# Kernel tuning notes

Measured on AMD Instinct MI355X. Metric: run time of the kernel, lower is better.

The kernel has to match this reference:

```python
import jax, jax.numpy as jnp
import numpy as np

Z_DIM = 1          # coord column zeroed before coalescing (module default)
GRID = 512         # max coordinate value per column (exclusive)


def setup_inputs() -> dict:
    key = jax.random.key(0)
    k1, k2 = jax.random.split(key)
    N, C = 400000, 128
    features = jax.random.normal(k1, (N, C), dtype=jnp.float32)
    coords = jax.random.randint(k2, (N, 4), 0, GRID, dtype=jnp.int32)
    return {"features": features, "coords": coords}


def reference(features, coords):
    # features: [N, C] float, coords: [N, 4] int32
    N = features.shape[0]
    # Zero the z column (BEV flattening), as in flatten_coords[:, z_dim] = 0.
    # Since the z column is identically 0 after zeroing, coalescing the 4-col
    # coords is equivalent to keying on the remaining 3 columns.
    non_z = [i for i in range(4) if i != Z_DIM]
    c0 = coords[:, non_z[0]].astype(jnp.int32)
    c1 = coords[:, non_z[1]].astype(jnp.int32)
    c2 = coords[:, non_z[2]].astype(jnp.int32)
    lin_key = (c0 * GRID + c1) * GRID + c2  # < 512^3 < 2^31, fits int32

    # coalesce(): unique coords + scatter-add of [count | features]
    uniq, inv = jnp.unique(lin_key, size=N, fill_value=-1, return_inverse=True)
    ones = jnp.ones((N, 1), dtype=features.dtype)
    feat_with_cnt = jnp.concatenate([ones, features], axis=1)  # [N, C+1]
    sums = jax.ops.segment_sum(feat_with_cnt, inv.reshape(-1), num_segments=N)  # [N, C+1]

    cnt = sums[:, :1]
    out_features = sums[:, 1:] / jnp.maximum(cnt, 1.0)  # padded rows have cnt=0 -> stay 0

    # Decode unique keys back to 4-column coords (z column = 0).
    d2 = uniq % GRID
    rem = uniq // GRID
    d1 = rem % GRID
    d0 = rem // GRID
    zeros = jnp.zeros_like(d0)
    cols = [None] * 4
    cols[Z_DIM] = zeros
    cols[non_z[0]] = d0
    cols[non_z[1]] = d1
    cols[non_z[2]] = d2
    out_coords = jnp.stack(cols, axis=1).astype(jnp.int32)  # [N, 4], padded rows negative

    return out_features, out_coords, cnt[:, 0]
```

## Files before the change

kernel.cpp:

```cpp
#include <hip/hip_runtime.h>


#define NWORDS      (1u << 22)
#define SCAN_BLOCKS 1024
#define WPB         (NWORDS / SCAN_BLOCKS)
#define WPT         (WPB / 256)

__device__ __forceinline__ unsigned key_of(const int* __restrict__ coords, int i) {
    int c0 = coords[(size_t)i * 4 + 0];
    int c1 = coords[(size_t)i * 4 + 2];
    int c2 = coords[(size_t)i * 4 + 3];
    return ((unsigned)c0 << 18) | ((unsigned)c1 << 9) | (unsigned)c2;
}

__global__ void k_build(const int* __restrict__ coords, unsigned* __restrict__ bitmap, int N) {
    int i = blockIdx.x * blockDim.x + threadIdx.x;
    if (i >= N) return;
    unsigned key = key_of(coords, i);
    atomicOr(&bitmap[key >> 5], 1u << (key & 31u));
}

__global__ void k_scan1(const unsigned* __restrict__ bitmap, unsigned* __restrict__ blockSums) {
    __shared__ unsigned sd[256];
    const uint4* bm = (const uint4*)(bitmap + (size_t)blockIdx.x * WPB + (size_t)threadIdx.x * WPT);
    unsigned s = 0;
#pragma unroll
    for (int k = 0; k < WPT / 4; ++k) {
        uint4 v = bm[k];
        s += __popc(v.x) + __popc(v.y) + __popc(v.z) + __popc(v.w);
    }
    sd[threadIdx.x] = s;
    __syncthreads();
    for (int off = 128; off > 0; off >>= 1) {
        if ((int)threadIdx.x < off) sd[threadIdx.x] += sd[threadIdx.x + off];
        __syncthreads();
    }
    if (threadIdx.x == 0) blockSums[blockIdx.x] = sd[0];
}

__global__ void k_scan2(const unsigned* __restrict__ blockSums, unsigned* __restrict__ blockOffsets) {
    __shared__ unsigned sd[SCAN_BLOCKS];
    int t = threadIdx.x;
    unsigned v = blockSums[t];
    sd[t] = v;
    __syncthreads();
    for (int off = 1; off < SCAN_BLOCKS; off <<= 1) {
        unsigned add = (t >= off) ? sd[t - off] : 0u;
        __syncthreads();
        sd[t] += add;
        __syncthreads();
    }
    blockOffsets[t] = sd[t] - v;
}

__global__ void k_scan3(const unsigned* __restrict__ bitmap,
                        const unsigned* __restrict__ blockOffsets,
                        unsigned* __restrict__ offsets) {
    __shared__ unsigned sd[256];
    size_t base = (size_t)blockIdx.x * WPB + (size_t)threadIdx.x * WPT;
    const uint4* bm = (const uint4*)(bitmap + base);
    unsigned pc[WPT];
    unsigned s = 0;
#pragma unroll
    for (int k = 0; k < WPT / 4; ++k) {
        uint4 v = bm[k];
        pc[k * 4 + 0] = __popc(v.x);
        pc[k * 4 + 1] = __popc(v.y);
        pc[k * 4 + 2] = __popc(v.z);
        pc[k * 4 + 3] = __popc(v.w);
        s += pc[k * 4] + pc[k * 4 + 1] + pc[k * 4 + 2] + pc[k * 4 + 3];
    }
    int t = threadIdx.x;
    sd[t] = s;
    __syncthreads();
    for (int off = 1; off < 256; off <<= 1) {
        unsigned add = (t >= off) ? sd[t - off] : 0u;
        __syncthreads();
        sd[t] += add;
        __syncthreads();
    }
    unsigned run = blockOffsets[blockIdx.x] + sd[t] - s;
#pragma unroll
    for (int k = 0; k < WPT; ++k) {
        offsets[base + k] = run;
        run += pc[k];
    }
}

__global__ void k_fill(float4* __restrict__ outc, int N) {
    int i = blockIdx.x * blockDim.x + threadIdx.x;
    if (i >= N) return;
    outc[i] = make_float4(-1.f, 0.f, 511.f, 511.f);
}

__global__ void k_enum(const unsigned* __restrict__ bitmap,
                       const unsigned* __restrict__ offsets,
                       float4* __restrict__ outc) {
    unsigned w = blockIdx.x * blockDim.x + threadIdx.x;
    unsigned bits = bitmap[w];
    if (!bits) return;
    unsigned row = offsets[w];
    while (bits) {
        int b = __ffs(bits) - 1;
        unsigned key = (w << 5) | (unsigned)b;
        float d0 = (float)(key >> 18);
        float d1 = (float)((key >> 9) & 511u);
        float d2 = (float)(key & 511u);
        outc[row] = make_float4(d0, 0.f, d1, d2);
        ++row;
        bits &= bits - 1u;
    }
}

__global__ void k_seg(const int* __restrict__ coords,
                      const unsigned* __restrict__ bitmap,
                      const unsigned* __restrict__ offsets,
                      unsigned* __restrict__ seg,
                      float* __restrict__ cnt, int N) {
    int i = blockIdx.x * blockDim.x + threadIdx.x;
    if (i >= N) return;
    unsigned key = key_of(coords, i);
    unsigned w = key >> 5, b = key & 31u;
    unsigned s = offsets[w] + __popc(bitmap[w] & ((1u << b) - 1u));
    seg[i] = s;
    atomicAdd(&cnt[s], 1.0f);
}

__global__ void k_zero(const float* __restrict__ cnt, float4* __restrict__ feat, int N) {
    int r = blockIdx.x * blockDim.x + threadIdx.x;
    if (r >= N) return;
    if (cnt[r] != 1.0f) {
        float4 z = make_float4(0.f, 0.f, 0.f, 0.f);
#pragma unroll
        for (int k = 0; k < 32; ++k) feat[(size_t)r * 32 + k] = z;
    }
}

__global__ void k_scatter(const float4* __restrict__ fin,
                          const unsigned* __restrict__ seg,
                          const float* __restrict__ cnt,
                          float4* __restrict__ fout, int N) {
    int gid = blockIdx.x * blockDim.x + threadIdx.x;
    int elem = gid >> 5;
    int c4 = gid & 31;
    if (elem >= N) return;
    unsigned s = seg[elem];
    float cv = cnt[s];
    float4 v = fin[(size_t)elem * 32 + c4];
    if (cv == 1.0f) {
        fout[(size_t)s * 32 + c4] = v;
    } else {
        float inv = 1.0f / cv;
        float* p = (float*)&fout[(size_t)s * 32 + c4];
        atomicAdd(p + 0, v.x * inv);
        atomicAdd(p + 1, v.y * inv);
        atomicAdd(p + 2, v.z * inv);
        atomicAdd(p + 3, v.w * inv);
    }
}

extern "C" void kernel_launch(void* const* d_in, const int* in_sizes, int n_in,
                              void* d_out, int out_size, void* d_ws, size_t ws_size,
                              hipStream_t stream) {
    const float4* feat_in = (const float4*)d_in[0];
    const int* coords = (const int*)d_in[1];
    int N = in_sizes[1] / 4;

    float* out = (float*)d_out;
    float* out_feat = out;
    float4* out_coords = (float4*)(out + (size_t)N * 128);
    float* out_cnt = out + (size_t)N * 132;

    unsigned* bitmap = (unsigned*)d_out;
    unsigned* offsets = bitmap + NWORDS;

    unsigned* seg = (unsigned*)d_ws;
    unsigned* blockSums = seg + N;
    unsigned* blockOffsets = blockSums + SCAN_BLOCKS;

    int nb = (N + 255) / 256;

    hipMemsetAsync(bitmap, 0, (size_t)NWORDS * 4, stream);
    hipMemsetAsync(out_cnt, 0, (size_t)N * 4, stream);

    k_build<<<nb, 256, 0, stream>>>(coords, bitmap, N);
    k_scan1<<<SCAN_BLOCKS, 256, 0, stream>>>(bitmap, blockSums);
    k_scan2<<<1, SCAN_BLOCKS, 0, stream>>>(blockSums, blockOffsets);
    k_scan3<<<SCAN_BLOCKS, 256, 0, stream>>>(bitmap, blockOffsets, offsets);
    k_fill<<<nb, 256, 0, stream>>>(out_coords, N);
    k_enum<<<NWORDS / 256, 256, 0, stream>>>(bitmap, offsets, out_coords);
    k_seg<<<nb, 256, 0, stream>>>(coords, bitmap, offsets, seg, out_cnt, N);
    k_zero<<<nb, 256, 0, stream>>>(out_cnt, (float4*)out_feat, N);
    k_scatter<<<(int)(((size_t)N * 32 + 255) / 256), 256, 0, stream>>>(
        feat_in, seg, out_cnt, (float4*)out_feat, N);
}
```

Before: 168.7 us.

## Fuse enumeration into scan, replace scatter with gather plus duplicate atomics

Fuses the coordinate enumeration into the final scan kernel and drops the separate fill kernel. Padding coords are now written inside the new gather kernel, using a total-unique count saved by the second scan. Keys are cached during the build pass, and an inverse map from unique row to source element lets singleton rows be copied by a coalesced gather. Only duplicate rows still use per-element atomic adds, now one thread per element looping over channels. The bitmap and offsets move from the output buffer to the workspace, which needs a larger workspace. The rewrite removes the zeroing pass and the full scatter, at the cost of an extra dependent pass over the output.

```diff
diff --git a/kernel.cpp b/kernel.cpp
--- a/kernel.cpp
+++ b/kernel.cpp
@@ -13,10 +13,12 @@
     return ((unsigned)c0 << 18) | ((unsigned)c1 << 9) | (unsigned)c2;
 }
 
-__global__ void k_build(const int* __restrict__ coords, unsigned* __restrict__ bitmap, int N) {
+__global__ void k_build(const int* __restrict__ coords, unsigned* __restrict__ bitmap,
+                        unsigned* __restrict__ keys, int N) {
     int i = blockIdx.x * blockDim.x + threadIdx.x;
     if (i >= N) return;
     unsigned key = key_of(coords, i);
+    keys[i] = key;
     atomicOr(&bitmap[key >> 5], 1u << (key & 31u));
 }
 
@@ -38,7 +40,9 @@
     if (threadIdx.x == 0) blockSums[blockIdx.x] = sd[0];
 }
 
-__global__ void k_scan2(const unsigned* __restrict__ blockSums, unsigned* __restrict__ blockOffsets) {
+__global__ void k_scan2(const unsigned* __restrict__ blockSums,
+                        unsigned* __restrict__ blockOffsets,
+                        unsigned* __restrict__ totalM) {
     __shared__ unsigned sd[SCAN_BLOCKS];
     int t = threadIdx.x;
     unsigned v = blockSums[t];
@@ -51,24 +55,23 @@
         __syncthreads();
     }
     blockOffsets[t] = sd[t] - v;
+    if (t == SCAN_BLOCKS - 1) totalM[0] = sd[t];
 }
 
-__global__ void k_scan3(const unsigned* __restrict__ bitmap,
-                        const unsigned* __restrict__ blockOffsets,
-                        unsigned* __restrict__ offsets) {
+__global__ void k_scan3enum(const unsigned* __restrict__ bitmap,
+                            const unsigned* __restrict__ blockOffsets,
+                            unsigned* __restrict__ offsets,
+                            float4* __restrict__ outc) {
     __shared__ unsigned sd[256];
     size_t base = (size_t)blockIdx.x * WPB + (size_t)threadIdx.x * WPT;
     const uint4* bm = (const uint4*)(bitmap + base);
-    unsigned pc[WPT];
+    unsigned w[WPT];
     unsigned s = 0;
 #pragma unroll
     for (int k = 0; k < WPT / 4; ++k) {
         uint4 v = bm[k];
-        pc[k * 4 + 0] = __popc(v.x);
-        pc[k * 4 + 1] = __popc(v.y);
-        pc[k * 4 + 2] = __popc(v.z);
-        pc[k * 4 + 3] = __popc(v.w);
-        s += pc[k * 4] + pc[k * 4 + 1] + pc[k * 4 + 2] + pc[k * 4 + 3];
+        w[k * 4 + 0] = v.x; w[k * 4 + 1] = v.y; w[k * 4 + 2] = v.z; w[k * 4 + 3] = v.w;
+        s += __popc(v.x) + __popc(v.y) + __popc(v.z) + __popc(v.w);
     }
     int t = threadIdx.x;
     sd[t] = s;
@@ -83,79 +86,74 @@
 #pragma unroll
     for (int k = 0; k < WPT; ++k) {
         offsets[base + k] = run;
-        run += pc[k];
+        unsigned bits = w[k];
+        while (bits) {
+            int b = __ffs(bits) - 1;
+            unsigned key = ((unsigned)(base + k) << 5) | (unsigned)b;
+            outc[run] = make_float4((float)(key >> 18), 0.f,
+                                    (float)((key >> 9) & 511u), (float)(key & 511u));
+            ++run;
+            bits &= bits - 1u;
+        }
     }
 }
 
-__global__ void k_fill(float4* __restrict__ outc, int N) {
+__global__ void k_seg(const unsigned* __restrict__ keys,
+                      const unsigned* __restrict__ bitmap,
+                      const unsigned* __restrict__ offsets,
+                      unsigned* __restrict__ seg,
+                      unsigned* __restrict__ srcElem,
+                      float* __restrict__ cnt, int N) {
     int i = blockIdx.x * blockDim.x + threadIdx.x;
     if (i >= N) return;
-    outc[i] = make_float4(-1.f, 0.f, 511.f, 511.f);
+    unsigned key = keys[i];
+    unsigned w = key >> 5, b = key & 31u;
+    unsigned s = offsets[w] + __popc(bitmap[w] & ((1u << b) - 1u));
+    seg[i] = s;
+    srcElem[s] = i;
+    atomicAdd(&cnt[s], 1.0f);
 }
 
-__global__ void k_enum(const unsigned* __restrict__ bitmap,
-                       const unsigned* __restrict__ offsets,
-                       float4* __restrict__ outc) {
-    unsigned w = blockIdx.x * blockDim.x + threadIdx.x;
-    unsigned bits = bitmap[w];
-    if (!bits) return;
-    unsigned row = offsets[w];
-    while (bits) {
-        int b = __ffs(bits) - 1;
-        unsigned key = (w << 5) | (unsigned)b;
-        float d0 = (float)(key >> 18);
-        float d1 = (float)((key >> 9) & 511u);
-        float d2 = (float)(key & 511u);
-        outc[row] = make_float4(d0, 0.f, d1, d2);
-        ++row;
-        bits &= bits - 1u;
+__global__ void k_gather(const float4* __restrict__ fin,
+                         const unsigned* __restrict__ srcElem,
+                         const float* __restrict__ cnt,
+                         const unsigned* __restrict__ totalM,
+                         float4* __restrict__ fout,
+                         float4* __restrict__ outc, int N) {
+    int gid = blockIdx.x * blockDim.x + threadIdx.x;
+    int r = gid >> 5;
+    if (r >= N) return;
+    int c4 = gid & 31;
+    float cv = cnt[r];
+    float4 v = make_float4(0.f, 0.f, 0.f, 0.f);
+    if (cv == 1.0f) {
+        unsigned e = srcElem[r];
+        v = fin[(size_t)e * 32 + c4];
+    }
+    fout[(size_t)r * 32 + c4] = v;
+    if (c4 == 0 && (unsigned)r >= totalM[0]) {
+        outc[r] = make_float4(-1.f, 0.f, 511.f, 511.f);
     }
 }
 
-__global__ void k_seg(const int* __restrict__ coords,
-                      const unsigned* __restrict__ bitmap,
-                      const unsigned* __restrict__ offsets,
-                      unsigned* __restrict__ seg,
-                      float* __restrict__ cnt, int N) {
+__global__ void k_dup(const float4* __restrict__ fin,
+                      const unsigned* __restrict__ seg,
+                      const float* __restrict__ cnt,
+                      float4* __restrict__ fout, int N) {
     int i = blockIdx.x * blockDim.x + threadIdx.x;
     if (i >= N) return;
-    unsigned key = key_of(coords, i);
-    unsigned w = key >> 5, b = key & 31u;
-    unsigned s = offsets[w] + __popc(bitmap[w] & ((1u << b) - 1u));
-    seg[i] = s;
-    atomicAdd(&cnt[s], 1.0f);
-}
-
-__global__ void k_zero(const float* __restrict__ cnt, float4* __restrict__ feat, int N) {
-    int r = blockIdx.x * blockDim.x + threadIdx.x;
-    if (r >= N) return;
-    if (cnt[r] != 1.0f) {
-        float4 z = make_float4(0.f, 0.f, 0.f, 0.f);
-#pragma unroll
-        for (int k = 0; k < 32; ++k) feat[(size_t)r * 32 + k] = z;
-    }
-}
-
-__global__ void k_scatter(const float4* __restrict__ fin,
-                          const unsigned* __restrict__ seg,
-                          const float* __restrict__ cnt,
-                          float4* __restrict__ fout, int N) {
-    int gid = blockIdx.x * blockDim.x + threadIdx.x;
-    int elem = gid >> 5;
-    int c4 = gid & 31;
-    if (elem >= N) return;
-    unsigned s = seg[elem];
+    unsigned s = seg[i];
     float cv = cnt[s];
-    float4 v = fin[(size_t)elem * 32 + c4];
-    if (cv == 1.0f) {
-        fout[(size_t)s * 32 + c4] = v;
-    } else {
-        float inv = 1.0f / cv;
-        float* p = (float*)&fout[(size_t)s * 32 + c4];
-        atomicAdd(p + 0, v.x * inv);
-        atomicAdd(p + 1, v.y * inv);
-        atomicAdd(p + 2, v.z * inv);
-        atomicAdd(p + 3, v.w * inv);
+    if (cv == 1.0f) return;
+    float inv = 1.0f / cv;
+    float* dst = (float*)(fout + (size_t)s * 32);
+#pragma unroll 4
+    for (int c4 = 0; c4 < 32; ++c4) {
+        float4 v = fin[(size_t)i * 32 + c4];
+        atomicAdd(dst + c4 * 4 + 0, v.x * inv);
+        atomicAdd(dst + c4 * 4 + 1, v.y * inv);
+        atomicAdd(dst + c4 * 4 + 2, v.z * inv);
+        atomicAdd(dst + c4 * 4 + 3, v.w * inv);
     }
 }
 
@@ -171,26 +169,26 @@
     float4* out_coords = (float4*)(out + (size_t)N * 128);
     float* out_cnt = out + (size_t)N * 132;
 
-    unsigned* bitmap = (unsigned*)d_out;
+    unsigned* bitmap = (unsigned*)d_ws;
     unsigned* offsets = bitmap + NWORDS;
-
-    unsigned* seg = (unsigned*)d_ws;
-    unsigned* blockSums = seg + N;
+    unsigned* keys = offsets + NWORDS;
+    unsigned* seg = keys + N;
+    unsigned* srcElem = seg + N;
+    unsigned* blockSums = srcElem + N;
     unsigned* blockOffsets = blockSums + SCAN_BLOCKS;
+    unsigned* totalM = blockOffsets + SCAN_BLOCKS;
 
     int nb = (N + 255) / 256;
 
     hipMemsetAsync(bitmap, 0, (size_t)NWORDS * 4, stream);
     hipMemsetAsync(out_cnt, 0, (size_t)N * 4, stream);
 
-    k_build<<<nb, 256, 0, stream>>>(coords, bitmap, N);
+    k_build<<<nb, 256, 0, stream>>>(coords, bitmap, keys, N);
     k_scan1<<<SCAN_BLOCKS, 256, 0, stream>>>(bitmap, blockSums);
-    k_scan2<<<1, SCAN_BLOCKS, 0, stream>>>(blockSums, blockOffsets);
-    k_scan3<<<SCAN_BLOCKS, 256, 0, stream>>>(bitmap, blockOffsets, offsets);
-    k_fill<<<nb, 256, 0, stream>>>(out_coords, N);
-    k_enum<<<NWORDS / 256, 256, 0, stream>>>(bitmap, offsets, out_coords);
-    k_seg<<<nb, 256, 0, stream>>>(coords, bitmap, offsets, seg, out_cnt, N);
-    k_zero<<<nb, 256, 0, stream>>>(out_cnt, (float4*)out_feat, N);
-    k_scatter<<<(int)(((size_t)N * 32 + 255) / 256), 256, 0, stream>>>(
-        feat_in, seg, out_cnt, (float4*)out_feat, N);
+    k_scan2<<<1, SCAN_BLOCKS, 0, stream>>>(blockSums, blockOffsets, totalM);
+    k_scan3enum<<<SCAN_BLOCKS, 256, 0, stream>>>(bitmap, blockOffsets, offsets, out_coords);
+    k_seg<<<nb, 256, 0, stream>>>(keys, bitmap, offsets, seg, srcElem, out_cnt, N);
+    k_gather<<<(int)(((size_t)N * 32 + 255) / 256), 256, 0, stream>>>(
+        feat_in, srcElem, out_cnt, totalM, (float4*)out_feat, out_coords, N);
+    k_dup<<<nb, 256, 0, stream>>>(feat_in, seg, out_cnt, (float4*)out_feat, N);
 }
```

Result: slower. 201.5 us (+19.4%).
